# Kernel optimization log

Hardware: AMD Instinct MI355X
Metric: run time of the kernel (lower is better)

Reference implementation:

```python
import jax, jax.numpy as jnp
import numpy as np

B, T, I, H = 32768, 50, 2, 32  # batch, seq_len, input_size, hidden_size


def setup_inputs() -> dict:
    key = jax.random.key(0)
    ks = jax.random.split(key, 7)
    return {
        "x": jax.random.normal(ks[0], (B, T, I), dtype=jnp.float32),
        "W_ih": jax.random.normal(ks[1], (4 * H, I), dtype=jnp.float32) * 0.1,
        "W_hh": jax.random.normal(ks[2], (4 * H, H), dtype=jnp.float32) * 0.1,
        "b_ih": jax.random.normal(ks[3], (4 * H,), dtype=jnp.float32) * 0.1,
        "b_hh": jax.random.normal(ks[4], (4 * H,), dtype=jnp.float32) * 0.1,
        "W_out": jax.random.normal(ks[5], (1, H), dtype=jnp.float32) * 0.1,
        "b_out": jax.random.normal(ks[6], (1,), dtype=jnp.float32) * 0.1,
        "h0": jnp.zeros((B, H), dtype=jnp.float32),
        "c0": jnp.zeros((B, H), dtype=jnp.float32),
    }


def reference(x, W_ih, W_hh, b_ih, b_hh, W_out, b_out, h0, c0):
    # Precompute input projection for all timesteps: [B, T, 4H]
    xg = jnp.einsum("bti,gi->btg", x, W_ih) + b_ih + b_hh

    def step(carry, xg_t):
        h, c = carry  # [B, H] each
        gates = xg_t + h @ W_hh.T  # [B, 4H]
        i, f, g, o = jnp.split(gates, 4, axis=-1)  # PyTorch gate order i,f,g,o
        i = jax.nn.sigmoid(i)
        f = jax.nn.sigmoid(f)
        g = jnp.tanh(g)
        o = jax.nn.sigmoid(o)
        c = f * c + i * g
        h = o * jnp.tanh(c)
        return (h, c), h

    (_, _), hs = jax.lax.scan(step, (h0, c0), jnp.swapaxes(xg, 0, 1))  # hs: [T, B, H]
    r_out = jnp.swapaxes(hs, 0, 1)  # [B, T, H]
    results = r_out @ W_out.T + b_out  # [B, T, 1]
    return results.reshape(-1, 50, 1)
```

## Files before the change

### kernel.cpp

```cpp
#include <hip/hip_runtime.h>


#define TS 50
#define XSTR 51
#define CL 14.0f
#define WPB 4

typedef short short8 __attribute__((ext_vector_type(8)));
typedef float f32x4 __attribute__((ext_vector_type(4)));
typedef float f32x2 __attribute__((ext_vector_type(2)));

__device__ __forceinline__ float fast_exp2(float x) {
    return __builtin_amdgcn_exp2f(x);
}
__device__ __forceinline__ float fast_rcp(float x) {
    return __builtin_amdgcn_rcpf(x);
}
__device__ __forceinline__ f32x2 pexp(f32x2 z) {
    f32x2 r; r.x = fast_exp2(z.x); r.y = fast_exp2(z.y); return r;
}
__device__ __forceinline__ f32x2 prcp(f32x2 v) {
    f32x2 r; r.x = fast_rcp(v.x); r.y = fast_rcp(v.y); return r;
}
__device__ __forceinline__ f32x2 vmin2(f32x2 v, float s) {
    f32x2 r; r.x = fminf(v.x, s); r.y = fminf(v.y, s); return r;
}
__device__ __forceinline__ unsigned split_pack(float v) {
    unsigned u   = __float_as_uint(v);
    float    res = v - __uint_as_float(u & 0xffff0000u);
    return __builtin_amdgcn_perm(__float_as_uint(res), u, 0x07060302u);
}
__device__ __forceinline__ unsigned lo_pair(unsigned a, unsigned b) {
    return __builtin_amdgcn_perm(b, a, 0x05040100u);
}
__device__ __forceinline__ unsigned hi_pair(unsigned a, unsigned b) {
    return __builtin_amdgcn_perm(b, a, 0x07060302u);
}
__device__ __forceinline__ void pack2(float a, float b,
                                      unsigned &whi, unsigned &wlo) {
    unsigned h, l;
    asm("v_cvt_pk_bf16_f32 %0, %1, %2" : "=v"(h) : "v"(a), "v"(b));
    float ra = a - __uint_as_float(h << 16);
    float rb = b - __uint_as_float(h & 0xffff0000u);
    asm("v_cvt_pk_bf16_f32 %0, %1, %2" : "=v"(l) : "v"(ra), "v"(rb));
    whi = h; wlo = l;
}

union U4S8 { uint4 v; short8 s; unsigned u[4]; };

__global__ __launch_bounds__(256, 2)
void lsnn_kernel(const float* __restrict__ x,
                 const float* __restrict__ W_ih,
                 const float* __restrict__ W_hh,
                 const float* __restrict__ b_ih,
                 const float* __restrict__ b_hh,
                 const float* __restrict__ W_out,
                 const float* __restrict__ b_out,
                 const float* __restrict__ h0,
                 const float* __restrict__ c0,
                 float* __restrict__ out)
{
    __shared__ __align__(16) unsigned xa0[WPB][16 * XSTR];
    __shared__ __align__(16) unsigned xa1[WPB][16 * XSTR];
    __shared__ __align__(16) unsigned xa2[WPB][16 * XSTR];
    __shared__ __align__(16) float    out_lds[WPB][16 * TS];

    const int  tid  = threadIdx.x;
    const int  g_w  = tid >> 6;
    const int  lane = tid & 63;
    const int  u0   = lane & 15;
    const int  q    = lane >> 4;
    const long b0   = ((long)blockIdx.x * WPB + g_w) * 16;

    unsigned* x0w = xa0[g_w];
    unsigned* x1w = xa1[g_w];
    unsigned* x2w = xa2[g_w];
    float*    ow  = out_lds[g_w];

    for (int i = lane; i < 800; i += 64) {
        int row = i / 50, t = i - row * 50;
        float2 v = *(const float2*)(x + (b0 + row) * 100 + 2 * t);
        unsigned a0 = split_pack(v.x), a1 = split_pack(v.y);
        x0w[row * XSTR + t] = a0;
        x1w[row * XSTR + t] = a1;
        x2w[row * XSTR + t] = lo_pair(a0, a1);
    }

    const float L2E = 1.4426950408889634f;
    const float SG  = 2.0f * L2E;

    short8 Awh[8], Awl[8], Aci[8];
    #pragma unroll
    for (int n = 0; n < 8; ++n) {
        const int   g  = n & 3, ub = n >> 2;
        const float s  = (g == 2) ? SG : -L2E;
        const int   R  = g * 32 + ub * 16 + u0;
        const float* wr = W_hh + R * 32;
        U4S8 uh, ul;
        #pragma unroll
        for (int p = 0; p < 4; ++p) {
            unsigned p0 = split_pack(wr[q * 4 + p]      * s);
            unsigned p1 = split_pack(wr[q * 4 + p + 16] * s);
            uh.u[p] = lo_pair(p0, p1);
            ul.u[p] = hi_pair(p0, p1);
        }
        Awh[n] = uh.s;  Awl[n] = ul.s;
        U4S8 ux;
        if (q == 0) {
            unsigned s0 = split_pack(W_ih[R * 2 + 0] * s);
            unsigned s1 = split_pack(W_ih[R * 2 + 1] * s);
            unsigned sb = split_pack((b_ih[R] + b_hh[R]) * s);
            ux.u[0] = lo_pair(s0, s0);
            ux.u[1] = lo_pair(s1, s1);
            ux.u[2] = hi_pair(s0, s1);
            ux.u[3] = sb;
        } else {
            ux.u[0] = 0u; ux.u[1] = 0u; ux.u[2] = 0u; ux.u[3] = 0u;
        }
        Aci[n] = ux.s;
    }
    short8 Awoh, Awol;
    {
        U4S8 uh, ul;
        #pragma unroll
        for (int p = 0; p < 4; ++p) {
            unsigned p0 = split_pack(W_out[q * 4 + p]);
            unsigned p1 = split_pack(W_out[q * 4 + p + 16]);
            uh.u[p] = lo_pair(p0, p1);
            ul.u[p] = hi_pair(p0, p1);
        }
        Awoh = uh.s;  Awol = ul.s;
    }
    const float bout = b_out[0];

    U4S8 Bhh, Bhl;
    {
        const float* hp = h0 + (b0 + u0) * 32 + q * 4;
        float4 ha = *(const float4*)hp;
        float4 hb = *(const float4*)(hp + 16);
        pack2(ha.x, hb.x, Bhh.u[0], Bhl.u[0]);
        pack2(ha.y, hb.y, Bhh.u[1], Bhl.u[1]);
        pack2(ha.z, hb.z, Bhh.u[2], Bhl.u[2]);
        pack2(ha.w, hb.w, Bhh.u[3], Bhl.u[3]);
    }
    f32x2 cst2[4];
    #pragma unroll
    for (int ub = 0; ub < 2; ++ub)
        #pragma unroll
        for (int rr = 0; rr < 2; ++rr)
            cst2[ub * 2 + rr] =
                *(const f32x2*)(c0 + (b0 + u0) * 32 + ub * 16 + q * 4 + 2 * rr);

    const f32x4 ZV = {0.f, 0.f, 0.f, 0.f};
    const int xbase = u0 * XSTR;

    unsigned xw0 = x0w[xbase], xw1 = x1w[xbase], xw2 = x2w[xbase];

    if (((blockIdx.x ^ (blockIdx.x >> 8)) & 1) != 0)
        __builtin_amdgcn_s_sleep(35);

    #pragma unroll 1
    for (int t = 0; t < TS; ++t) {
        U4S8 Bx;
        Bx.u[0] = xw0;  Bx.u[1] = xw1;  Bx.u[2] = xw2;
        Bx.u[3] = 0x3f803f80u;
        if (t + 1 < TS) {
            xw0 = x0w[xbase + t + 1];
            xw1 = x1w[xbase + t + 1];
            xw2 = x2w[xbase + t + 1];
        }

        if (t > 0) {
            f32x4 aw = ZV;
            aw = __builtin_amdgcn_mfma_f32_16x16x32_bf16(Awoh, Bhh.s, aw, 0, 0, 0);
            aw = __builtin_amdgcn_mfma_f32_16x16x32_bf16(Awoh, Bhl.s, aw, 0, 0, 0);
            aw = __builtin_amdgcn_mfma_f32_16x16x32_bf16(Awol, Bhh.s, aw, 0, 0, 0);
            if (q == 0) ow[u0 * TS + (t - 1)] = aw[0] + bout;
        }

        f32x4 acc[8];
        #pragma unroll
        for (int n = 0; n < 8; ++n)
            acc[n] = __builtin_amdgcn_mfma_f32_16x16x32_bf16(Aci[n], Bx.s, ZV, 0, 0, 0);
        #pragma unroll
        for (int n = 0; n < 8; ++n) {
            acc[n] = __builtin_amdgcn_mfma_f32_16x16x32_bf16(Awh[n], Bhh.s, acc[n], 0, 0, 0);
            acc[n] = __builtin_amdgcn_mfma_f32_16x16x32_bf16(Awh[n], Bhl.s, acc[n], 0, 0, 0);
            acc[n] = __builtin_amdgcn_mfma_f32_16x16x32_bf16(Awl[n], Bhh.s, acc[n], 0, 0, 0);
        }

        f32x2 Bv2[4], Cv2[4], Ev2[4], P12[4], PP2[4];
        #pragma unroll
        for (int ub = 0; ub < 2; ++ub) {
            #pragma unroll
            for (int rr = 0; rr < 2; ++rr) {
                const int gi = ub * 2 + rr, nb = ub * 4;
                f32x2 zi = {acc[nb + 0][2*rr], acc[nb + 0][2*rr + 1]};
                f32x2 zf = {acc[nb + 1][2*rr], acc[nb + 1][2*rr + 1]};
                f32x2 zg = vmin2((f32x2){acc[nb + 2][2*rr], acc[nb + 2][2*rr + 1]}, CL);
                f32x2 zo = {acc[nb + 3][2*rr], acc[nb + 3][2*rr + 1]};
                f32x2 Av = pexp(zi);
                Bv2[gi]  = pexp(zg);
                Ev2[gi]  = pexp(zf);
                Cv2[gi]  = pexp(zo);
                f32x2 Ap = 1.0f + Av;
                P12[gi] = Ap * Bv2[gi] + Ap;
                PP2[gi] = P12[gi] * Ev2[gi] + P12[gi];
            }
        }
        f32x2 R2[4];
        #pragma unroll
        for (int bb = 0; bb < 2; ++bb) {
            f32x2 pr = PP2[2*bb] * PP2[2*bb + 1];
            f32x2 ri = prcp(pr);
            R2[2*bb]     = PP2[2*bb + 1] * ri;
            R2[2*bb + 1] = PP2[2*bb]     * ri;
        }
        f32x2 Dv2[4], Q2[4];
        #pragma unroll
        for (int gi = 0; gi < 4; ++gi) {
            f32x2 fv = P12[gi] * R2[gi];
            f32x2 t2 = Ev2[gi] * R2[gi] + R2[gi];
            f32x2 ig = Bv2[gi] * t2 - t2;
            f32x2 c  = fv * cst2[gi] + ig;
            cst2[gi] = c;
            f32x2 zc = vmin2(c * SG, CL);
            Dv2[gi] = pexp(zc);
            f32x2 Qp = 1.0f + Cv2[gi];
            Q2[gi]  = Qp * Dv2[gi] + Qp;
        }
        f32x2 RQ2[4];
        #pragma unroll
        for (int bb = 0; bb < 2; ++bb) {
            f32x2 qr = Q2[2*bb] * Q2[2*bb + 1];
            f32x2 ri = prcp(qr);
            RQ2[2*bb]     = Q2[2*bb + 1] * ri;
            RQ2[2*bb + 1] = Q2[2*bb]     * ri;
        }
        float hub[2][4];
        #pragma unroll
        for (int gi = 0; gi < 4; ++gi) {
            f32x2 h2 = Dv2[gi] * RQ2[gi] - RQ2[gi];
            hub[gi >> 1][2 * (gi & 1)]     = h2.x;
            hub[gi >> 1][2 * (gi & 1) + 1] = h2.y;
        }
        #pragma unroll
        for (int p = 0; p < 4; ++p)
            pack2(hub[0][p], hub[1][p], Bhh.u[p], Bhl.u[p]);
    }

    {
        f32x4 aw = {0.f, 0.f, 0.f, 0.f};
        aw = __builtin_amdgcn_mfma_f32_16x16x32_bf16(Awoh, Bhh.s, aw, 0, 0, 0);
        aw = __builtin_amdgcn_mfma_f32_16x16x32_bf16(Awoh, Bhl.s, aw, 0, 0, 0);
        aw = __builtin_amdgcn_mfma_f32_16x16x32_bf16(Awol, Bhh.s, aw, 0, 0, 0);
        if (q == 0) ow[u0 * TS + 49] = aw[0] + bout;
    }

    {
        float4* od = (float4*)(out + b0 * 50);
        const float4* os = (const float4*)ow;
        for (int i = lane; i < 200; i += 64) od[i] = os[i];
    }
}

extern "C" void kernel_launch(void* const* d_in, const int* in_sizes, int n_in,
                              void* d_out, int out_size, void* d_ws, size_t ws_size,
                              hipStream_t stream) {
    const float* x     = (const float*)d_in[0];
    const float* W_ih  = (const float*)d_in[1];
    const float* W_hh  = (const float*)d_in[2];
    const float* b_ih  = (const float*)d_in[3];
    const float* b_hh  = (const float*)d_in[4];
    const float* W_out = (const float*)d_in[5];
    const float* b_out = (const float*)d_in[6];
    const float* h0    = (const float*)d_in[7];
    const float* c0    = (const float*)d_in[8];
    float* out = (float*)d_out;

    dim3 grid(32768 / (16 * WPB)), block(64 * WPB);
    lsnn_kernel<<<grid, block, 0, stream>>>(x, W_ih, W_hh, b_ih, b_hh,
                                            W_out, b_out, h0, c0, out);
}
```

Before: 151.3 us.

## Process two independent 16-row batch tiles per wave and drop LDS x staging

Each wave now handles 32 batch rows as two interleaved independent recurrences, giving the scheduler two dependency chains to overlap MFMA and transcendental latency within one wave. The x input is no longer staged and pre-split in LDS; each step loads its float2 directly from global memory one step ahead and splits it in registers. The grid is halved, launch bounds drop to one block per SIMD set, and the staggered s_sleep is removed. This raises register pressure and reduces wave count, and adds per-step global loads with a small stride.

```diff
diff --git a/kernel.cpp b/kernel.cpp
--- a/kernel.cpp
+++ b/kernel.cpp
@@ -2,7 +2,6 @@
 
 
 #define TS 50
-#define XSTR 51
 #define CL 14.0f
 #define WPB 4
 
@@ -48,7 +47,7 @@
 
 union U4S8 { uint4 v; short8 s; unsigned u[4]; };
 
-__global__ __launch_bounds__(256, 2)
+__global__ __launch_bounds__(256, 1)
 void lsnn_kernel(const float* __restrict__ x,
                  const float* __restrict__ W_ih,
                  const float* __restrict__ W_hh,
@@ -60,31 +59,16 @@
                  const float* __restrict__ c0,
                  float* __restrict__ out)
 {
-    __shared__ __align__(16) unsigned xa0[WPB][16 * XSTR];
-    __shared__ __align__(16) unsigned xa1[WPB][16 * XSTR];
-    __shared__ __align__(16) unsigned xa2[WPB][16 * XSTR];
-    __shared__ __align__(16) float    out_lds[WPB][16 * TS];
+    __shared__ __align__(16) float out_lds[WPB][32 * TS];
 
     const int  tid  = threadIdx.x;
     const int  g_w  = tid >> 6;
     const int  lane = tid & 63;
     const int  u0   = lane & 15;
     const int  q    = lane >> 4;
-    const long b0   = ((long)blockIdx.x * WPB + g_w) * 16;
-
-    unsigned* x0w = xa0[g_w];
-    unsigned* x1w = xa1[g_w];
-    unsigned* x2w = xa2[g_w];
-    float*    ow  = out_lds[g_w];
-
-    for (int i = lane; i < 800; i += 64) {
-        int row = i / 50, t = i - row * 50;
-        float2 v = *(const float2*)(x + (b0 + row) * 100 + 2 * t);
-        unsigned a0 = split_pack(v.x), a1 = split_pack(v.y);
-        x0w[row * XSTR + t] = a0;
-        x1w[row * XSTR + t] = a1;
-        x2w[row * XSTR + t] = lo_pair(a0, a1);
-    }
+    const long wbase = ((long)blockIdx.x * WPB + g_w) * 32;
+
+    float* ow = out_lds[g_w];
 
     const float L2E = 1.4426950408889634f;
     const float SG  = 2.0f * L2E;
@@ -133,134 +117,138 @@
     }
     const float bout = b_out[0];
 
-    U4S8 Bhh, Bhl;
-    {
-        const float* hp = h0 + (b0 + u0) * 32 + q * 4;
+    U4S8 Bhh[2], Bhl[2];
+    f32x2 cst2[2][4];
+    float2 xcur[2];
+    #pragma unroll
+    for (int pb = 0; pb < 2; ++pb) {
+        const long row = wbase + pb * 16 + u0;
+        const float* hp = h0 + row * 32 + q * 4;
         float4 ha = *(const float4*)hp;
         float4 hb = *(const float4*)(hp + 16);
-        pack2(ha.x, hb.x, Bhh.u[0], Bhl.u[0]);
-        pack2(ha.y, hb.y, Bhh.u[1], Bhl.u[1]);
-        pack2(ha.z, hb.z, Bhh.u[2], Bhl.u[2]);
-        pack2(ha.w, hb.w, Bhh.u[3], Bhl.u[3]);
-    }
-    f32x2 cst2[4];
-    #pragma unroll
-    for (int ub = 0; ub < 2; ++ub)
-        #pragma unroll
-        for (int rr = 0; rr < 2; ++rr)
-            cst2[ub * 2 + rr] =
-                *(const f32x2*)(c0 + (b0 + u0) * 32 + ub * 16 + q * 4 + 2 * rr);
+        pack2(ha.x, hb.x, Bhh[pb].u[0], Bhl[pb].u[0]);
+        pack2(ha.y, hb.y, Bhh[pb].u[1], Bhl[pb].u[1]);
+        pack2(ha.z, hb.z, Bhh[pb].u[2], Bhl[pb].u[2]);
+        pack2(ha.w, hb.w, Bhh[pb].u[3], Bhl[pb].u[3]);
+        #pragma unroll
+        for (int ub = 0; ub < 2; ++ub)
+            #pragma unroll
+            for (int rr = 0; rr < 2; ++rr)
+                cst2[pb][ub * 2 + rr] =
+                    *(const f32x2*)(c0 + row * 32 + ub * 16 + q * 4 + 2 * rr);
+        xcur[pb] = *(const float2*)(x + row * 100);
+    }
 
     const f32x4 ZV = {0.f, 0.f, 0.f, 0.f};
-    const int xbase = u0 * XSTR;
-
-    unsigned xw0 = x0w[xbase], xw1 = x1w[xbase], xw2 = x2w[xbase];
-
-    if (((blockIdx.x ^ (blockIdx.x >> 8)) & 1) != 0)
-        __builtin_amdgcn_s_sleep(35);
 
     #pragma unroll 1
     for (int t = 0; t < TS; ++t) {
-        U4S8 Bx;
-        Bx.u[0] = xw0;  Bx.u[1] = xw1;  Bx.u[2] = xw2;
-        Bx.u[3] = 0x3f803f80u;
-        if (t + 1 < TS) {
-            xw0 = x0w[xbase + t + 1];
-            xw1 = x1w[xbase + t + 1];
-            xw2 = x2w[xbase + t + 1];
-        }
-
-        if (t > 0) {
-            f32x4 aw = ZV;
-            aw = __builtin_amdgcn_mfma_f32_16x16x32_bf16(Awoh, Bhh.s, aw, 0, 0, 0);
-            aw = __builtin_amdgcn_mfma_f32_16x16x32_bf16(Awoh, Bhl.s, aw, 0, 0, 0);
-            aw = __builtin_amdgcn_mfma_f32_16x16x32_bf16(Awol, Bhh.s, aw, 0, 0, 0);
-            if (q == 0) ow[u0 * TS + (t - 1)] = aw[0] + bout;
-        }
-
-        f32x4 acc[8];
-        #pragma unroll
-        for (int n = 0; n < 8; ++n)
-            acc[n] = __builtin_amdgcn_mfma_f32_16x16x32_bf16(Aci[n], Bx.s, ZV, 0, 0, 0);
-        #pragma unroll
-        for (int n = 0; n < 8; ++n) {
-            acc[n] = __builtin_amdgcn_mfma_f32_16x16x32_bf16(Awh[n], Bhh.s, acc[n], 0, 0, 0);
-            acc[n] = __builtin_amdgcn_mfma_f32_16x16x32_bf16(Awh[n], Bhl.s, acc[n], 0, 0, 0);
-            acc[n] = __builtin_amdgcn_mfma_f32_16x16x32_bf16(Awl[n], Bhh.s, acc[n], 0, 0, 0);
-        }
-
-        f32x2 Bv2[4], Cv2[4], Ev2[4], P12[4], PP2[4];
-        #pragma unroll
-        for (int ub = 0; ub < 2; ++ub) {
-            #pragma unroll
-            for (int rr = 0; rr < 2; ++rr) {
-                const int gi = ub * 2 + rr, nb = ub * 4;
-                f32x2 zi = {acc[nb + 0][2*rr], acc[nb + 0][2*rr + 1]};
-                f32x2 zf = {acc[nb + 1][2*rr], acc[nb + 1][2*rr + 1]};
-                f32x2 zg = vmin2((f32x2){acc[nb + 2][2*rr], acc[nb + 2][2*rr + 1]}, CL);
-                f32x2 zo = {acc[nb + 3][2*rr], acc[nb + 3][2*rr + 1]};
-                f32x2 Av = pexp(zi);
-                Bv2[gi]  = pexp(zg);
-                Ev2[gi]  = pexp(zf);
-                Cv2[gi]  = pexp(zo);
-                f32x2 Ap = 1.0f + Av;
-                P12[gi] = Ap * Bv2[gi] + Ap;
-                PP2[gi] = P12[gi] * Ev2[gi] + P12[gi];
-            }
-        }
-        f32x2 R2[4];
-        #pragma unroll
-        for (int bb = 0; bb < 2; ++bb) {
-            f32x2 pr = PP2[2*bb] * PP2[2*bb + 1];
-            f32x2 ri = prcp(pr);
-            R2[2*bb]     = PP2[2*bb + 1] * ri;
-            R2[2*bb + 1] = PP2[2*bb]     * ri;
-        }
-        f32x2 Dv2[4], Q2[4];
-        #pragma unroll
-        for (int gi = 0; gi < 4; ++gi) {
-            f32x2 fv = P12[gi] * R2[gi];
-            f32x2 t2 = Ev2[gi] * R2[gi] + R2[gi];
-            f32x2 ig = Bv2[gi] * t2 - t2;
-            f32x2 c  = fv * cst2[gi] + ig;
-            cst2[gi] = c;
-            f32x2 zc = vmin2(c * SG, CL);
-            Dv2[gi] = pexp(zc);
-            f32x2 Qp = 1.0f + Cv2[gi];
-            Q2[gi]  = Qp * Dv2[gi] + Qp;
-        }
-        f32x2 RQ2[4];
-        #pragma unroll
-        for (int bb = 0; bb < 2; ++bb) {
-            f32x2 qr = Q2[2*bb] * Q2[2*bb + 1];
-            f32x2 ri = prcp(qr);
-            RQ2[2*bb]     = Q2[2*bb + 1] * ri;
-            RQ2[2*bb + 1] = Q2[2*bb]     * ri;
-        }
-        float hub[2][4];
-        #pragma unroll
-        for (int gi = 0; gi < 4; ++gi) {
-            f32x2 h2 = Dv2[gi] * RQ2[gi] - RQ2[gi];
-            hub[gi >> 1][2 * (gi & 1)]     = h2.x;
-            hub[gi >> 1][2 * (gi & 1) + 1] = h2.y;
-        }
-        #pragma unroll
-        for (int p = 0; p < 4; ++p)
-            pack2(hub[0][p], hub[1][p], Bhh.u[p], Bhl.u[p]);
+        #pragma unroll
+        for (int pb = 0; pb < 2; ++pb) {
+            unsigned a0 = split_pack(xcur[pb].x);
+            unsigned a1 = split_pack(xcur[pb].y);
+            U4S8 Bx;
+            Bx.u[0] = a0;
+            Bx.u[1] = a1;
+            Bx.u[2] = lo_pair(a0, a1);
+            Bx.u[3] = 0x3f803f80u;
+            if (t + 1 < TS)
+                xcur[pb] = *(const float2*)
+                    (x + (wbase + pb * 16 + u0) * 100 + 2 * (t + 1));
+
+            if (t > 0) {
+                f32x4 aw = ZV;
+                aw = __builtin_amdgcn_mfma_f32_16x16x32_bf16(Awoh, Bhh[pb].s, aw, 0, 0, 0);
+                aw = __builtin_amdgcn_mfma_f32_16x16x32_bf16(Awoh, Bhl[pb].s, aw, 0, 0, 0);
+                aw = __builtin_amdgcn_mfma_f32_16x16x32_bf16(Awol, Bhh[pb].s, aw, 0, 0, 0);
+                if (q == 0) ow[(pb * 16 + u0) * TS + (t - 1)] = aw[0] + bout;
+            }
+
+            f32x4 acc[8];
+            #pragma unroll
+            for (int n = 0; n < 8; ++n)
+                acc[n] = __builtin_amdgcn_mfma_f32_16x16x32_bf16(Aci[n], Bx.s, ZV, 0, 0, 0);
+            #pragma unroll
+            for (int n = 0; n < 8; ++n) {
+                acc[n] = __builtin_amdgcn_mfma_f32_16x16x32_bf16(Awh[n], Bhh[pb].s, acc[n], 0, 0, 0);
+                acc[n] = __builtin_amdgcn_mfma_f32_16x16x32_bf16(Awh[n], Bhl[pb].s, acc[n], 0, 0, 0);
+                acc[n] = __builtin_amdgcn_mfma_f32_16x16x32_bf16(Awl[n], Bhh[pb].s, acc[n], 0, 0, 0);
+            }
+
+            f32x2 Bv2[4], Cv2[4], Ev2[4], P12[4], PP2[4];
+            #pragma unroll
+            for (int ub = 0; ub < 2; ++ub) {
+                #pragma unroll
+                for (int rr = 0; rr < 2; ++rr) {
+                    const int gi = ub * 2 + rr, nb = ub * 4;
+                    f32x2 zi = {acc[nb + 0][2*rr], acc[nb + 0][2*rr + 1]};
+                    f32x2 zf = {acc[nb + 1][2*rr], acc[nb + 1][2*rr + 1]};
+                    f32x2 zg = vmin2((f32x2){acc[nb + 2][2*rr], acc[nb + 2][2*rr + 1]}, CL);
+                    f32x2 zo = {acc[nb + 3][2*rr], acc[nb + 3][2*rr + 1]};
+                    f32x2 Av = pexp(zi);
+                    Bv2[gi]  = pexp(zg);
+                    Ev2[gi]  = pexp(zf);
+                    Cv2[gi]  = pexp(zo);
+                    f32x2 Ap = 1.0f + Av;
+                    P12[gi] = Ap * Bv2[gi] + Ap;
+                    PP2[gi] = P12[gi] * Ev2[gi] + P12[gi];
+                }
+            }
+            f32x2 R2[4];
+            #pragma unroll
+            for (int bb = 0; bb < 2; ++bb) {
+                f32x2 pr = PP2[2*bb] * PP2[2*bb + 1];
+                f32x2 ri = prcp(pr);
+                R2[2*bb]     = PP2[2*bb + 1] * ri;
+                R2[2*bb + 1] = PP2[2*bb]     * ri;
+            }
+            f32x2 Dv2[4], Q2[4];
+            #pragma unroll
+            for (int gi = 0; gi < 4; ++gi) {
+                f32x2 fv = P12[gi] * R2[gi];
+                f32x2 t2 = Ev2[gi] * R2[gi] + R2[gi];
+                f32x2 ig = Bv2[gi] * t2 - t2;
+                f32x2 c  = fv * cst2[pb][gi] + ig;
+                cst2[pb][gi] = c;
+                f32x2 zc = vmin2(c * SG, CL);
+                Dv2[gi] = pexp(zc);
+                f32x2 Qp = 1.0f + Cv2[gi];
+                Q2[gi]  = Qp * Dv2[gi] + Qp;
+            }
+            f32x2 RQ2[4];
+            #pragma unroll
+            for (int bb = 0; bb < 2; ++bb) {
+                f32x2 qr = Q2[2*bb] * Q2[2*bb + 1];
+                f32x2 ri = prcp(qr);
+                RQ2[2*bb]     = Q2[2*bb + 1] * ri;
+                RQ2[2*bb + 1] = Q2[2*bb]     * ri;
+            }
+            float hub[2][4];
+            #pragma unroll
+            for (int gi = 0; gi < 4; ++gi) {
+                f32x2 h2 = Dv2[gi] * RQ2[gi] - RQ2[gi];
+                hub[gi >> 1][2 * (gi & 1)]     = h2.x;
+                hub[gi >> 1][2 * (gi & 1) + 1] = h2.y;
+            }
+            #pragma unroll
+            for (int p = 0; p < 4; ++p)
+                pack2(hub[0][p], hub[1][p], Bhh[pb].u[p], Bhl[pb].u[p]);
+        }
+    }
+
+    #pragma unroll
+    for (int pb = 0; pb < 2; ++pb) {
+        f32x4 aw = {0.f, 0.f, 0.f, 0.f};
+        aw = __builtin_amdgcn_mfma_f32_16x16x32_bf16(Awoh, Bhh[pb].s, aw, 0, 0, 0);
+        aw = __builtin_amdgcn_mfma_f32_16x16x32_bf16(Awoh, Bhl[pb].s, aw, 0, 0, 0);
+        aw = __builtin_amdgcn_mfma_f32_16x16x32_bf16(Awol, Bhh[pb].s, aw, 0, 0, 0);
+        if (q == 0) ow[(pb * 16 + u0) * TS + 49] = aw[0] + bout;
     }
 
     {
-        f32x4 aw = {0.f, 0.f, 0.f, 0.f};
-        aw = __builtin_amdgcn_mfma_f32_16x16x32_bf16(Awoh, Bhh.s, aw, 0, 0, 0);
-        aw = __builtin_amdgcn_mfma_f32_16x16x32_bf16(Awoh, Bhl.s, aw, 0, 0, 0);
-        aw = __builtin_amdgcn_mfma_f32_16x16x32_bf16(Awol, Bhh.s, aw, 0, 0, 0);
-        if (q == 0) ow[u0 * TS + 49] = aw[0] + bout;
-    }
-
-    {
-        float4* od = (float4*)(out + b0 * 50);
+        float4* od = (float4*)(out + wbase * 50);
         const float4* os = (const float4*)ow;
-        for (int i = lane; i < 200; i += 64) od[i] = os[i];
+        for (int i = lane; i < 400; i += 64) od[i] = os[i];
     }
 }
 
@@ -278,7 +266,7 @@
     const float* c0    = (const float*)d_in[8];
     float* out = (float*)d_out;
 
-    dim3 grid(32768 / (16 * WPB)), block(64 * WPB);
+    dim3 grid(32768 / (32 * WPB)), block(64 * WPB);
     lsnn_kernel<<<grid, block, 0, stream>>>(x, W_ih, W_hh, b_ih, b_hh,
                                             W_out, b_out, h0, c0, out);
 }
```

After: 157.9 us. 4.3% more time.
